# Kernel optimization log

Hardware: AMD Instinct MI355X
Metric: run time of the kernel (lower is better)

## Reference

```python
import jax, jax.numpy as jnp
import numpy as np

EPS = 0.0  # GINConv eps

def _gin_conv(x, edge_index, W1, b1, W2, b2, n_nodes):
    # GINConv: mlp((1+eps)*x + sum_{j in N(i)} x_j)
    src, dst = edge_index[0], edge_index[1]
    agg = jax.ops.segment_sum(x[src], dst, num_segments=n_nodes)  # [N, d]
    h = (1.0 + EPS) * x + agg
    h = jax.nn.relu(h @ W1 + b1)  # Linear -> Identity(BN off) -> ReLU
    return h @ W2 + b2            # second Linear


def setup_inputs() -> dict:
    key = jax.random.key(0)
    ks = jax.random.split(key, 10)
    N, E = 50000, 600000
    d_in, d_hid, d_out = 128, 256, 128
    x = jax.random.normal(ks[0], (N, d_in), dtype=jnp.float32)
    edge_index = jax.random.randint(ks[1], (2, E), 0, N, dtype=jnp.int64)

    def lin(k, fan_in, fan_out):
        bound = 1.0 / np.sqrt(fan_in)
        kw, kb = jax.random.split(k)
        W = jax.random.uniform(kw, (fan_in, fan_out), jnp.float32, -bound, bound)
        b = jax.random.uniform(kb, (fan_out,), jnp.float32, -bound, bound)
        return W, b

    W1a, b1a = lin(ks[2], d_in, d_hid)   # conv0 mlp: 128->256
    W2a, b2a = lin(ks[3], d_hid, d_hid)  # conv0 mlp: 256->256
    W1b, b1b = lin(ks[4], d_hid, d_hid)  # conv1 mlp: 256->256
    W2b, b2b = lin(ks[5], d_hid, d_out)  # conv1 mlp: 256->128
    return {"x": x, "W1a": W1a, "b1a": b1a, "W2a": W2a, "b2a": b2a,
            "W1b": W1b, "b1b": b1b, "W2b": W2b, "b2b": b2b,
            "edge_index": edge_index}


def reference(x, W1a, b1a, W2a, b2a, W1b, b1b, W2b, b2b, edge_index):
    n_nodes = x.shape[0]
    # layer 0: GINConv -> relu (use_bn=False; dropout is identity in eval)
    h = _gin_conv(x, edge_index, W1a, b1a, W2a, b2a, n_nodes)
    h = jax.nn.relu(h)
    # final GINConv (no activation after, per forward())
    return _gin_conv(h, edge_index, W1b, b1b, W2b, b2b, n_nodes)
```

## Files before the change

kernel.cpp:

```cpp
#include <hip/hip_runtime.h>


typedef __bf16 bf16x8 __attribute__((ext_vector_type(8)));
typedef float f32x4 __attribute__((ext_vector_type(4)));
typedef float f32x2 __attribute__((ext_vector_type(2)));
typedef unsigned short u16x4 __attribute__((ext_vector_type(4)));
typedef unsigned short u16x8 __attribute__((ext_vector_type(8)));
typedef unsigned int uint32;
typedef uint32 u32x4 __attribute__((ext_vector_type(4)));

__device__ __forceinline__ unsigned short f2bf(float f) {
  uint32 u = __builtin_bit_cast(uint32, f);
  u += 0x7FFFu + ((u >> 16) & 1u);
  return (unsigned short)(u >> 16);
}
__device__ __forceinline__ f32x2 bfpair(uint32 w) {
  f32x2 r;
  r.x = __builtin_bit_cast(float, w << 16);
  r.y = __builtin_bit_cast(float, w & 0xFFFF0000u);
  return r;
}

#define G2L16(gp, lp)                                                        \
  __builtin_amdgcn_global_load_lds(                                          \
      (const __attribute__((address_space(1))) void*)(gp),                   \
      (__attribute__((address_space(3))) void*)(lp), 16, 0, 0)

__global__ void hist(const int* __restrict__ eidx, int* __restrict__ deg, int E) {
  int e = blockIdx.x * blockDim.x + threadIdx.x;
  if (e < E) atomicAdd(&deg[eidx[e + E]], 1);
}

__global__ __launch_bounds__(256) void scan_all(
    const int* __restrict__ deg, int* __restrict__ offs, int* __restrict__ pos,
    int* __restrict__ aggr, int* __restrict__ incl, int* __restrict__ flg,
    int Nn, int nb) {
  __shared__ int sm[256];
  __shared__ int s_prefix;
  const int t = threadIdx.x;
  const int b = blockIdx.x;
  const int i = b * 256 + t;
  int v = (i < Nn) ? deg[i] : 0;
  sm[t] = v;
  __syncthreads();
#pragma unroll
  for (int off = 1; off < 256; off <<= 1) {
    int add = (t >= off) ? sm[t - off] : 0;
    __syncthreads();
    sm[t] += add;
    __syncthreads();
  }
  if (t == 255) {
    atomicExch(&aggr[b], sm[255]);
    atomicExch(&flg[b], 1);
  }
  if (b == 0) {
    for (int j = t; j < nb; j += 256)
      while (atomicAdd(&flg[j], 0) == 0) __builtin_amdgcn_s_sleep(1);
    __syncthreads();
    int a = (t < nb) ? atomicAdd(&aggr[t], 0) : 0;
    __shared__ int sb[256];
    sb[t] = a;
    __syncthreads();
#pragma unroll
    for (int off = 1; off < 256; off <<= 1) {
      int add = (t >= off) ? sb[t - off] : 0;
      __syncthreads();
      sb[t] += add;
      __syncthreads();
    }
    if (t < nb) atomicExch(&incl[t], sb[t]);
    __syncthreads();
    if (t == 0) atomicExch(&flg[nb], 1);
    if (t == 0) s_prefix = 0;
  } else {
    if (t == 0) {
      while (atomicAdd(&flg[nb], 0) == 0) __builtin_amdgcn_s_sleep(8);
      s_prefix = atomicAdd(&incl[b - 1], 0);
    }
  }
  __syncthreads();
  int ex = s_prefix + sm[t] - v;
  if (i < Nn) {
    offs[i] = ex;
    pos[i] = ex;
    if (i == Nn - 1) offs[Nn] = ex + v;
  }
}

__global__ void fill_csr(const int* __restrict__ eidx, int* __restrict__ pos,
                         int* __restrict__ esrc, int E) {
  int e = blockIdx.x * blockDim.x + threadIdx.x;
  if (e < E) {
    int s = eidx[e];
    int d = eidx[e + E];
    int p = atomicAdd(&pos[d], 1);
    esrc[p] = s;
  }
}

__global__ __launch_bounds__(256) void prep(
    int* __restrict__ zp, int zn,
    const float* __restrict__ x, unsigned short* __restrict__ xb, long long n4,
    const float* __restrict__ W1a, const float* __restrict__ W2a,
    const float* __restrict__ W1b, const float* __restrict__ W2b,
    unsigned short* __restrict__ w1t, unsigned short* __restrict__ w2t,
    unsigned short* __restrict__ w3t, unsigned short* __restrict__ w4t) {
  int zb = (zn + 255) >> 8;
  int b = blockIdx.x;
  int t = threadIdx.x;
  if (b < zb) {
    int i = b * 256 + t;
    if (i < zn) zp[i] = 0;
  } else if (b < zb + 768) {
    int i = (b - zb) * 256 + t;
    const float* W;
    unsigned short* WT;
    int K, N, j;
    if (i < 32768) {
      W = W1a; WT = w1t; K = 128; N = 256; j = i;
    } else if (i < 98304) {
      W = W2a; WT = w2t; K = 256; N = 256; j = i - 32768;
    } else if (i < 163840) {
      W = W1b; WT = w3t; K = 256; N = 256; j = i - 98304;
    } else {
      W = W2b; WT = w4t; K = 256; N = 128; j = i - 163840;
    }
    int k = j / N, n = j - k * N;
    WT[n * K + k] = f2bf(W[j]);
  } else {
    long long i = (long long)(b - zb - 768) * 256 + t;
    long long stride = (long long)(gridDim.x - zb - 768) * 256;
    for (; i < n4; i += stride) {
      float4 v = ((const float4*)x)[i];
      u16x4 o;
      o.x = f2bf(v.x); o.y = f2bf(v.y); o.z = f2bf(v.z); o.w = f2bf(v.w);
      ((u16x4*)xb)[i] = o;
    }
  }
}

template <int GRP>
__global__ __launch_bounds__(256) void agg_gather(
    unsigned short* __restrict__ out, const unsigned short* __restrict__ src,
    const int* __restrict__ offs, const int* __restrict__ esrc, int Nn) {
  constexpr int RS = GRP * 8;
  constexpr int GPB = 256 / GRP;
  const int gid = threadIdx.x / GRP;
  const int gl  = threadIdx.x % GRP;
  const unsigned short* sp = src + gl * 8;
  const int stride = gridDim.x * GPB;
  for (int node = blockIdx.x * GPB + gid; node < Nn; node += stride) {
    const int beg = offs[node];
    const int deg = offs[node + 1] - beg;
    f32x2 acc[4];
    {
      u32x4 w = *(const u32x4*)(sp + node * RS);
#pragma unroll
      for (int k = 0; k < 4; ++k) acc[k] = bfpair(w[k]);
    }
    int j = 0;
    for (; j + 8 <= deg; j += 8) {
      int idx[8];
#pragma unroll
      for (int u = 0; u < 8; ++u) idx[u] = esrc[beg + j + u];
#pragma unroll
      for (int u = 0; u < 8; ++u) {
        u32x4 w = *(const u32x4*)(sp + idx[u] * RS);
#pragma unroll
        for (int k = 0; k < 4; ++k) acc[k] += bfpair(w[k]);
      }
    }
    if (j < deg) {
#pragma unroll
      for (int u = 0; u < 8; ++u) {
        int jj = j + u;
        int e = beg + (jj < deg ? jj : deg - 1);
        float sel = (jj < deg) ? 1.f : 0.f;
        f32x2 fs = {sel, sel};
        int rv = esrc[e];
        u32x4 w = *(const u32x4*)(sp + rv * RS);
#pragma unroll
        for (int k = 0; k < 4; ++k) acc[k] += bfpair(w[k]) * fs;
      }
    }
    u16x8 o;
#pragma unroll
    for (int k = 0; k < 4; ++k) {
      o[2 * k] = f2bf(acc[k].x);
      o[2 * k + 1] = f2bf(acc[k].y);
    }
    *(u16x8*)(out + (size_t)node * RS + gl * 8) = o;
  }
}

template <int K1, int N2, bool OUT_BF16>
__global__ __launch_bounds__(256) void fused_mlp(
    const unsigned short* __restrict__ A,
    const unsigned short* __restrict__ BT1, const float* __restrict__ b1,
    const unsigned short* __restrict__ BT2, const float* __restrict__ b2,
    void* __restrict__ Cout, int M) {
  __shared__ unsigned short As[64 * 32];
  __shared__ unsigned short Bs[256 * 32];
  __shared__ unsigned short Ts[64 * 264];
  const int tid = threadIdx.x;
  const int wave = tid >> 6, lane = tid & 63;
  const int quad = lane >> 4, l16 = lane & 15;
  const int rowBase = blockIdx.x * 64;
  const int r16 = lane >> 2;
  const int kq = lane & 3;
  const int kqs = kq ^ ((r16 >> 1) & 3);
  const int sq = (quad ^ ((l16 >> 1) & 3)) * 8;

  long long arow = min(rowBase + wave * 16 + r16, M - 1);
  const unsigned short* ga = A + arow * K1 + kqs * 8;
  const unsigned short* gb = BT1 + (long long)(wave * 64 + r16) * K1 + kqs * 8;
  unsigned short* la = As + wave * 16 * 32;
  f32x4 acc[4][4] = {};
  for (int k0 = 0; k0 < K1; k0 += 32) {
    G2L16(ga, la);
    ga += 32;
#pragma unroll
    for (int c = 0; c < 4; ++c)
      G2L16(gb + (long long)(16 * c) * K1, Bs + (wave * 64 + 16 * c) * 32);
    gb += 32;
    __syncthreads();
    bf16x8 af[4], bfr[4];
#pragma unroll
    for (int mi = 0; mi < 4; ++mi)
      af[mi] = *(const bf16x8*)(As + (mi * 16 + l16) * 32 + sq);
#pragma unroll
    for (int ni = 0; ni < 4; ++ni)
      bfr[ni] = *(const bf16x8*)(Bs + (wave * 64 + ni * 16 + l16) * 32 + sq);
#pragma unroll
    for (int mi = 0; mi < 4; ++mi)
#pragma unroll
      for (int ni = 0; ni < 4; ++ni)
        acc[mi][ni] = __builtin_amdgcn_mfma_f32_16x16x32_bf16(
            af[mi], bfr[ni], acc[mi][ni], 0, 0, 0);
    __syncthreads();
  }
#pragma unroll
  for (int ni = 0; ni < 4; ++ni) {
    int col = wave * 64 + ni * 16 + l16;
    float bv = b1[col];
#pragma unroll
    for (int mi = 0; mi < 4; ++mi)
#pragma unroll
      for (int r = 0; r < 4; ++r) {
        int row = mi * 16 + quad * 4 + r;
        Ts[row * 264 + col] = f2bf(fmaxf(acc[mi][ni][r] + bv, 0.f));
      }
  }
  __syncthreads();

  constexpr int NI2 = N2 / 64;
  const int wcol = wave * (N2 / 4);
  const unsigned short* gb2 = BT2 + (long long)(wcol + r16) * 256 + kqs * 8;
  f32x4 acc2[4][NI2] = {};
  for (int k2 = 0; k2 < 256; k2 += 32) {
#pragma unroll
    for (int c = 0; c < NI2; ++c)
      G2L16(gb2 + (long long)(16 * c) * 256, Bs + (wcol + 16 * c) * 32);
    gb2 += 32;
    __syncthreads();
    bf16x8 af[4], bfr[NI2];
#pragma unroll
    for (int mi = 0; mi < 4; ++mi)
      af[mi] = *(const bf16x8*)(Ts + (mi * 16 + l16) * 264 + k2 + quad * 8);
#pragma unroll
    for (int ni = 0; ni < NI2; ++ni)
      bfr[ni] = *(const bf16x8*)(Bs + (wcol + ni * 16 + l16) * 32 + sq);
#pragma unroll
    for (int mi = 0; mi < 4; ++mi)
#pragma unroll
      for (int ni = 0; ni < NI2; ++ni)
        acc2[mi][ni] = __builtin_amdgcn_mfma_f32_16x16x32_bf16(
            af[mi], bfr[ni], acc2[mi][ni], 0, 0, 0);
    __syncthreads();
  }
#pragma unroll
  for (int ni = 0; ni < NI2; ++ni) {
    int col = wcol + ni * 16 + l16;
    float bv = b2[col];
#pragma unroll
    for (int mi = 0; mi < 4; ++mi)
#pragma unroll
      for (int r = 0; r < 4; ++r) {
        int row = rowBase + mi * 16 + quad * 4 + r;
        if (row < M) {
          float o = acc2[mi][ni][r] + bv;
          if (OUT_BF16)
            ((unsigned short*)Cout)[(long long)row * N2 + col] = f2bf(fmaxf(o, 0.f));
          else
            ((float*)Cout)[(long long)row * N2 + col] = o;
        }
      }
  }
}

extern "C" void kernel_launch(void* const* d_in, const int* in_sizes, int n_in,
                              void* d_out, int out_size, void* d_ws, size_t ws_size,
                              hipStream_t stream) {
  const float* x   = (const float*)d_in[0];
  const float* W1a = (const float*)d_in[1];
  const float* b1a = (const float*)d_in[2];
  const float* W2a = (const float*)d_in[3];
  const float* b2a = (const float*)d_in[4];
  const float* W1b = (const float*)d_in[5];
  const float* b1b = (const float*)d_in[6];
  const float* W2b = (const float*)d_in[7];
  const float* b2b = (const float*)d_in[8];
  const int*   ei  = (const int*)d_in[9];

  const int Nn = in_sizes[0] / 128;
  const int E  = in_sizes[9] / 2;
  float* out = (float*)d_out;

  const int nb = (Nn + 255) / 256;

  unsigned short* h   = (unsigned short*)d_ws;
  unsigned short* g0  = h  + (size_t)Nn * 256;
  unsigned short* g1  = g0 + (size_t)Nn * 128;
  unsigned short* xb  = g1 + (size_t)Nn * 256;
  unsigned short* w1t = xb + (size_t)Nn * 128;
  unsigned short* w2t = w1t + 256 * 128;
  unsigned short* w3t = w2t + 256 * 256;
  unsigned short* w4t = w3t + 256 * 256;
  int* deg  = (int*)(w4t + 128 * 256);
  int* flg  = deg + Nn;
  int* aggr = flg + nb + 1;
  int* incl = aggr + nb;
  int* offs = incl + nb;
  int* pos  = offs + Nn + 1;
  int* esrc = pos + Nn;

  dim3 blk(256);
  int zn = Nn + nb + 1;
  int zb = (zn + 255) / 256;

  prep<<<zb + 768 + 2048, blk, 0, stream>>>(deg, zn, x, xb,
                                            (long long)Nn * 128 / 4,
                                            W1a, W2a, W1b, W2b,
                                            w1t, w2t, w3t, w4t);
  hist<<<(E + 255) / 256, blk, 0, stream>>>(ei, deg, E);
  scan_all<<<nb, blk, 0, stream>>>(deg, offs, pos, aggr, incl, flg, Nn, nb);
  fill_csr<<<(E + 255) / 256, blk, 0, stream>>>(ei, pos, esrc, E);

  int mlpBlocks = (Nn + 63) / 64;

  agg_gather<16><<<2048, blk, 0, stream>>>(g0, xb, offs, esrc, Nn);
  fused_mlp<128, 256, true><<<mlpBlocks, blk, 0, stream>>>(
      g0, w1t, b1a, w2t, b2a, h, Nn);
  agg_gather<32><<<2048, blk, 0, stream>>>(g1, h, offs, esrc, Nn);
  fused_mlp<256, 128, false><<<mlpBlocks, blk, 0, stream>>>(
      g1, w3t, b1b, w4t, b2b, out, Nn);
}
```

Measured before the change: 292.4 us.

## Load MLP GEMM operands directly from global into registers, dropping LDS staging

The fused MLP kernel no longer stages A and weight tiles through shared memory with global_load_lds and per-k-step barriers. Each lane now reads its bf16x8 MFMA fragments straight from global memory (cached weights and activation rows), with the k loop unrolled by two. This removes the barriers and LDS traffic and frees shared memory for occupancy. The cost is that the A tile is re-read by all four waves and the weight rows by every block, all through L1/L2.

```diff
diff --git a/kernel.cpp b/kernel.cpp
--- a/kernel.cpp
+++ b/kernel.cpp
@@ -20,11 +20,6 @@
   r.y = __builtin_bit_cast(float, w & 0xFFFF0000u);
   return r;
 }
-
-#define G2L16(gp, lp)                                                        \
-  __builtin_amdgcn_global_load_lds(                                          \
-      (const __attribute__((address_space(1))) void*)(gp),                   \
-      (__attribute__((address_space(3))) void*)(lp), 16, 0, 0)
 
 __global__ void hist(const int* __restrict__ eidx, int* __restrict__ deg, int E) {
   int e = blockIdx.x * blockDim.x + threadIdx.x;
@@ -200,45 +195,38 @@
     const unsigned short* __restrict__ BT1, const float* __restrict__ b1,
     const unsigned short* __restrict__ BT2, const float* __restrict__ b2,
     void* __restrict__ Cout, int M) {
-  __shared__ unsigned short As[64 * 32];
-  __shared__ unsigned short Bs[256 * 32];
   __shared__ unsigned short Ts[64 * 264];
   const int tid = threadIdx.x;
   const int wave = tid >> 6, lane = tid & 63;
   const int quad = lane >> 4, l16 = lane & 15;
   const int rowBase = blockIdx.x * 64;
-  const int r16 = lane >> 2;
-  const int kq = lane & 3;
-  const int kqs = kq ^ ((r16 >> 1) & 3);
-  const int sq = (quad ^ ((l16 >> 1) & 3)) * 8;
-
-  long long arow = min(rowBase + wave * 16 + r16, M - 1);
-  const unsigned short* ga = A + arow * K1 + kqs * 8;
-  const unsigned short* gb = BT1 + (long long)(wave * 64 + r16) * K1 + kqs * 8;
-  unsigned short* la = As + wave * 16 * 32;
+
+  const unsigned short* ap[4];
+#pragma unroll
+  for (int mi = 0; mi < 4; ++mi) {
+    long long r = rowBase + mi * 16 + l16;
+    if (r > (long long)M - 1) r = M - 1;
+    ap[mi] = A + r * K1 + quad * 8;
+  }
+  const unsigned short* bp[4];
+#pragma unroll
+  for (int ni = 0; ni < 4; ++ni)
+    bp[ni] = BT1 + (long long)(wave * 64 + ni * 16 + l16) * K1 + quad * 8;
+
   f32x4 acc[4][4] = {};
+#pragma unroll 2
   for (int k0 = 0; k0 < K1; k0 += 32) {
-    G2L16(ga, la);
-    ga += 32;
-#pragma unroll
-    for (int c = 0; c < 4; ++c)
-      G2L16(gb + (long long)(16 * c) * K1, Bs + (wave * 64 + 16 * c) * 32);
-    gb += 32;
-    __syncthreads();
     bf16x8 af[4], bfr[4];
 #pragma unroll
-    for (int mi = 0; mi < 4; ++mi)
-      af[mi] = *(const bf16x8*)(As + (mi * 16 + l16) * 32 + sq);
-#pragma unroll
-    for (int ni = 0; ni < 4; ++ni)
-      bfr[ni] = *(const bf16x8*)(Bs + (wave * 64 + ni * 16 + l16) * 32 + sq);
+    for (int mi = 0; mi < 4; ++mi) af[mi] = *(const bf16x8*)(ap[mi] + k0);
+#pragma unroll
+    for (int ni = 0; ni < 4; ++ni) bfr[ni] = *(const bf16x8*)(bp[ni] + k0);
 #pragma unroll
     for (int mi = 0; mi < 4; ++mi)
 #pragma unroll
       for (int ni = 0; ni < 4; ++ni)
         acc[mi][ni] = __builtin_amdgcn_mfma_f32_16x16x32_bf16(
             af[mi], bfr[ni], acc[mi][ni], 0, 0, 0);
-    __syncthreads();
   }
 #pragma unroll
   for (int ni = 0; ni < 4; ++ni) {
@@ -256,28 +244,26 @@
 
   constexpr int NI2 = N2 / 64;
   const int wcol = wave * (N2 / 4);
-  const unsigned short* gb2 = BT2 + (long long)(wcol + r16) * 256 + kqs * 8;
+  const unsigned short* b2p[NI2];
+#pragma unroll
+  for (int ni = 0; ni < NI2; ++ni)
+    b2p[ni] = BT2 + (long long)(wcol + ni * 16 + l16) * 256 + quad * 8;
+
   f32x4 acc2[4][NI2] = {};
+#pragma unroll 2
   for (int k2 = 0; k2 < 256; k2 += 32) {
-#pragma unroll
-    for (int c = 0; c < NI2; ++c)
-      G2L16(gb2 + (long long)(16 * c) * 256, Bs + (wcol + 16 * c) * 32);
-    gb2 += 32;
-    __syncthreads();
     bf16x8 af[4], bfr[NI2];
 #pragma unroll
     for (int mi = 0; mi < 4; ++mi)
       af[mi] = *(const bf16x8*)(Ts + (mi * 16 + l16) * 264 + k2 + quad * 8);
 #pragma unroll
-    for (int ni = 0; ni < NI2; ++ni)
-      bfr[ni] = *(const bf16x8*)(Bs + (wcol + ni * 16 + l16) * 32 + sq);
+    for (int ni = 0; ni < NI2; ++ni) bfr[ni] = *(const bf16x8*)(b2p[ni] + k2);
 #pragma unroll
     for (int mi = 0; mi < 4; ++mi)
 #pragma unroll
       for (int ni = 0; ni < NI2; ++ni)
         acc2[mi][ni] = __builtin_amdgcn_mfma_f32_16x16x32_bf16(
             af[mi], bfr[ni], acc2[mi][ni], 0, 0, 0);
-    __syncthreads();
   }
 #pragma unroll
   for (int ni = 0; ni < NI2; ++ni) {
```

New measurement: 328.5 us. 1.12x slower.
